# Optimization experiments

Hardware: AMD Instinct MI355X
Metric: run time of the kernel (lower is better)

The kernel has to match this reference:

```python
import jax, jax.numpy as jnp
import numpy as np

N_BATCH, S, CH = 16384, 7, 30  # B*5+num_classes = 2*5+20
CO_COORD, CO_NOOBJ = 5.0, 0.5


def setup_inputs() -> dict:
    key = jax.random.key(0)
    k1, k2, k3 = jax.random.split(key, 3)
    preds = jax.random.uniform(k1, (N_BATCH, S, S, CH), dtype=jnp.float32)
    targets = jax.random.uniform(k2, (N_BATCH, S, S, CH), dtype=jnp.float32)
    obj = (jax.random.uniform(k3, (N_BATCH, S, S)) > 0.7).astype(jnp.float32)
    targets = targets.at[..., 4].set(obj * targets[..., 4] + obj * 1e-3)
    return {"preds": preds, "targets": targets}


def reference(preds, targets):
    # NOTE: faithful to the original torch code, including its bug where
    # coo_target is taken from preds (so box_target/class_target == the
    # predictions), making loc_loss and class_loss identically zero while
    # contain_loss compares pred confidence against (detached) IoU.
    N = preds.shape[0]
    P = preds.reshape(-1, CH)            # [NC, 30], NC = N*S*S
    T = targets.reshape(-1, CH)
    conf_t = T[:, 4]
    coo = (conf_t > 0).astype(preds.dtype)   # cells with object
    noo = (conf_t == 0).astype(preds.dtype)  # cells without object

    # --- no-object confidence loss (channels 4 and 9) ---
    nooobj_loss = jnp.sum(noo * ((P[:, 4] - T[:, 4]) ** 2 + (P[:, 9] - T[:, 9]) ** 2))

    # --- per-cell box matching (vectorized version of the python loop) ---
    boxes = P[:, :10].reshape(-1, 2, 5)       # [NC, 2, 5] predicted boxes
    xy = boxes[..., :2] / 14.0                # 14.0 == 2*S hardcoded upstream
    wh = boxes[..., 2:4]
    lt1 = xy - 0.5 * wh                       # [NC, 2, 2]
    rb1 = xy + 0.5 * wh
    tbox = boxes[:, 0]                        # box2 = box_target[i] == first pred box (bug)
    lt2 = tbox[:, :2] / 14.0 - 0.5 * tbox[:, 2:4]  # [NC, 2]
    rb2 = tbox[:, :2] / 14.0 + 0.5 * tbox[:, 2:4]

    ilt = jnp.maximum(lt1, lt2[:, None, :])
    irb = jnp.minimum(rb1, rb2[:, None, :])
    iwh = jnp.maximum(irb - ilt, 0.0)
    inter = iwh[..., 0] * iwh[..., 1]                    # [NC, 2]
    area1 = (rb1 - lt1)[..., 0] * (rb1 - lt1)[..., 1]    # [NC, 2]
    area2 = ((rb2 - lt2)[..., 0] * (rb2 - lt2)[..., 1])[:, None]
    iou = inter / (area1 + area2 - inter)                # [NC, 2]

    max_iou = jnp.max(iou, axis=1)                       # [NC]
    idx = jnp.argmax(iou, axis=1)                        # [NC] in {0,1}
    resp = jnp.take_along_axis(boxes, idx[:, None, None], axis=1)[:, 0]       # responsible box
    nresp = jnp.take_along_axis(boxes, (1 - idx)[:, None, None], axis=1)[:, 0]
    tgt_resp = resp  # box_target == box_pred due to the upstream bug

    # contain: pred conf vs detached IoU (original uses max_iou.data)
    contain_loss = jnp.sum(coo * (resp[:, 4] - jax.lax.stop_gradient(max_iou)) ** 2)
    # loc: identically zero given the bug, but computed faithfully
    loc_loss = (jnp.sum(coo[:, None] * (resp[:, :2] - tgt_resp[:, :2]) ** 2)
                + jnp.sum(coo[:, None] * (jnp.sqrt(resp[:, 2:4]) - jnp.sqrt(tgt_resp[:, 2:4])) ** 2))
    # not-responsible box: target conf zeroed
    not_contain_loss = jnp.sum(coo * nresp[:, 4] ** 2)
    # class loss: class_target also taken from preds (bug) -> zero
    cls = P[:, 10:]
    class_loss = jnp.sum(coo[:, None] * (cls - cls) ** 2)

    total = (CO_COORD * loc_loss + contain_loss + CO_NOOBJ * not_contain_loss
             + CO_NOOBJ * nooobj_loss + class_loss) / N
    return total
```

## Files before the change

kernel.cpp:

```cpp
#include <hip/hip_runtime.h>


#define TILE 256
#define NT   2

__device__ __forceinline__ float cell_loss(const float p[10], float t4, float t9) {
    float coo = (t4 > 0.0f) ? 1.0f : 0.0f;
    float noo = (t4 == 0.0f) ? 1.0f : 0.0f;

    float d4 = p[4] - t4;
    float d9 = p[9] - t9;
    float noo_term = noo * (d4 * d4 + d9 * d9);

    float lt2x = p[0] / 14.0f - 0.5f * p[2];
    float lt2y = p[1] / 14.0f - 0.5f * p[3];
    float rb2x = p[0] / 14.0f + 0.5f * p[2];
    float rb2y = p[1] / 14.0f + 0.5f * p[3];
    float area2 = (rb2x - lt2x) * (rb2y - lt2y);

    float iou[2];
    #pragma unroll
    for (int b = 0; b < 2; ++b) {
        float x = p[5 * b] / 14.0f;
        float y = p[5 * b + 1] / 14.0f;
        float w = p[5 * b + 2];
        float h = p[5 * b + 3];
        float lt1x = x - 0.5f * w, lt1y = y - 0.5f * h;
        float rb1x = x + 0.5f * w, rb1y = y + 0.5f * h;
        float iltx = fmaxf(lt1x, lt2x), ilty = fmaxf(lt1y, lt2y);
        float irbx = fminf(rb1x, rb2x), irby = fminf(rb1y, rb2y);
        float iwx = fmaxf(irbx - iltx, 0.0f);
        float iwy = fmaxf(irby - ilty, 0.0f);
        float inter = iwx * iwy;
        float area1 = (rb1x - lt1x) * (rb1y - lt1y);
        iou[b] = inter / (area1 + area2 - inter);
    }

    int idx;
    float max_iou;
    if (isnan(iou[0]))      { idx = 0; max_iou = iou[0]; }
    else if (isnan(iou[1])) { idx = 1; max_iou = iou[1]; }
    else                    { idx = (iou[1] > iou[0]) ? 1 : 0;
                              max_iou = fmaxf(iou[0], iou[1]); }

    float resp4  = p[5 * idx + 4];
    float nresp4 = p[5 * (1 - idx) + 4];
    float cdiff  = resp4 - max_iou;
    return coo * (cdiff * cdiff + 0.5f * nresp4 * nresp4) + 0.5f * noo_term;
}

struct TileRegs { float4 pv[3]; float4 tv[2]; };

__device__ __forceinline__ void issue_tile(const float* __restrict__ preds,
                                           const float* __restrict__ targets,
                                           long tile0, int tid, TileRegs& R) {
    const float4* gp = reinterpret_cast<const float4*>(preds + tile0 * 30);
    const float4* gt = reinterpret_cast<const float4*>(targets + tile0 * 30);
    #pragma unroll
    for (int k = 0; k < 3; ++k) {
        int L = tid + 256 * k;
        int pair = L / 6, rr = L - pair * 6;
        int r = (rr < 3) ? rr : rr + 4;
        R.pv[k] = gp[pair * 15 + r];
    }
    #pragma unroll
    for (int k = 0; k < 2; ++k) {
        int L = tid + 256 * k;
        int pair = L / 4, rr = L & 3;
        int r = (rr < 2) ? rr + 1 : rr + 6;
        R.tv[k] = gt[pair * 15 + r];
    }
}

__device__ __forceinline__ void write_tile(float4* smem4, float2* S2, float* Tc,
                                           int tid, const TileRegs& R) {
    #pragma unroll
    for (int k = 0; k < 3; ++k) {
        int L = tid + 256 * k;
        int pair = L / 6, rr = L - pair * 6;
        if (rr == 2)      S2[(pair * 5 + 2) * 2]     = make_float2(R.pv[k].x, R.pv[k].y);
        else if (rr == 3) S2[(pair * 5 + 2) * 2 + 1] = make_float2(R.pv[k].z, R.pv[k].w);
        else { int slot = (rr < 2) ? rr : rr - 1; smem4[pair * 5 + slot] = R.pv[k]; }
    }
    #pragma unroll
    for (int k = 0; k < 2; ++k) {
        int L = tid + 256 * k;
        int pair = L / 4, rr = L & 3;
        float v = (rr == 0) ? R.tv[k].x : (rr == 1) ? R.tv[k].y
                : (rr == 2) ? R.tv[k].z : R.tv[k].w;
        Tc[pair * 4 + rr] = v;
    }
}

__device__ __forceinline__ float compute_tile(const float2* S2, const float* Tc, int tid) {
    float p[10];
    #pragma unroll
    for (int k = 0; k < 5; ++k) {
        float2 q = S2[5 * tid + k];
        p[2 * k]     = q.x;
        p[2 * k + 1] = q.y;
    }
    return cell_loss(p, Tc[2 * tid], Tc[2 * tid + 1]);
}

__global__ __launch_bounds__(256) void yolo_loss_kernel(
    const float* __restrict__ preds,
    const float* __restrict__ targets,
    float* __restrict__ partials,
    int ncells)
{
    __shared__ float4 smem4[768];
    __shared__ float  warp_sums[4];
    float2* S2 = reinterpret_cast<float2*>(smem4);
    float*  Tc = reinterpret_cast<float*>(smem4 + 640);

    const int tid = threadIdx.x;
    const long tA = (long)blockIdx.x * (NT * TILE);
    const long tB = tA + TILE;
    float contrib = 0.0f;

    if (tB + TILE <= ncells) {
        TileRegs A, B;
        issue_tile(preds, targets, tA, tid, A);
        write_tile(smem4, S2, Tc, tid, A);
        __syncthreads();
        issue_tile(preds, targets, tB, tid, B);
        contrib = compute_tile(S2, Tc, tid);
        __syncthreads();
        write_tile(smem4, S2, Tc, tid, B);
        __syncthreads();
        contrib += compute_tile(S2, Tc, tid);
    } else {
        #pragma unroll
        for (int t = 0; t < NT; ++t) {
            long cell = tA + (long)t * TILE + tid;
            if (cell < ncells) {
                long base = cell * 30;
                float p[10];
                #pragma unroll
                for (int k = 0; k < 5; ++k) {
                    float2 v = *reinterpret_cast<const float2*>(preds + base + 2 * k);
                    p[2 * k] = v.x;
                    p[2 * k + 1] = v.y;
                }
                contrib += cell_loss(p, targets[base + 4], targets[base + 9]);
            }
        }
    }

    #pragma unroll
    for (int off = 32; off > 0; off >>= 1)
        contrib += __shfl_down(contrib, off, 64);

    int lane = tid & 63;
    int wid  = tid >> 6;
    if (lane == 0) warp_sums[wid] = contrib;
    __syncthreads();

    if (tid == 0) {
        partials[blockIdx.x] = warp_sums[0] + warp_sums[1] + warp_sums[2] + warp_sums[3];
    }
}

__global__ __launch_bounds__(256) void yolo_reduce_kernel(
    const float* __restrict__ partials,
    float* __restrict__ out,
    int nparts)
{
    __shared__ float warp_sums[4];
    const int tid = threadIdx.x;

    float s = 0.0f;
    for (int i = tid; i < nparts; i += 256)
        s += partials[i];

    #pragma unroll
    for (int off = 32; off > 0; off >>= 1)
        s += __shfl_down(s, off, 64);

    int lane = tid & 63;
    int wid  = tid >> 6;
    if (lane == 0) warp_sums[wid] = s;
    __syncthreads();

    if (tid == 0) {
        out[0] = (warp_sums[0] + warp_sums[1] + warp_sums[2] + warp_sums[3])
                 * (1.0f / 16384.0f);
    }
}

extern "C" void kernel_launch(void* const* d_in, const int* in_sizes, int n_in,
                              void* d_out, int out_size, void* d_ws, size_t ws_size,
                              hipStream_t stream) {
    const float* preds   = (const float*)d_in[0];
    const float* targets = (const float*)d_in[1];
    float* out = (float*)d_out;
    float* partials = (float*)d_ws;

    int ncells = in_sizes[0] / 30;
    int grid = (ncells + NT * TILE - 1) / (NT * TILE);

    yolo_loss_kernel<<<grid, 256, 0, stream>>>(preds, targets, partials, ncells);
    yolo_reduce_kernel<<<1, 256, 0, stream>>>(partials, out, grid);
}
```

Baseline: 36.56 us.

## Stage tiles via direct global-to-LDS loads and issue both tiles upfront

Replaces the register-staged global loads and scattered LDS writes with `__builtin_amdgcn_global_load_lds` 16-byte transfers that land data in LDS in load order. Both tiles are now issued before a single barrier, and compute reads the raw interleaved layout with an even/odd-thread split. The goal is to cut VGPR staging, LDS write instructions and intermediate barriers while putting more loads in flight. In exchange, LDS use per block grows from about 12KB to 40KB, which can limit resident blocks per CU, and an extra barrier is added before the reduction reuses the shared buffer.

```diff
diff --git a/kernel.cpp b/kernel.cpp
--- a/kernel.cpp
+++ b/kernel.cpp
@@ -3,6 +3,13 @@
 
 #define TILE 256
 #define NT   2
+
+__device__ __forceinline__ void gld16(const void* g, void* lds) {
+    __builtin_amdgcn_global_load_lds(
+        (const __attribute__((address_space(1))) void*)g,
+        (__attribute__((address_space(3))) void*)lds,
+        16, 0, 0);
+}
 
 __device__ __forceinline__ float cell_loss(const float p[10], float t4, float t9) {
     float coo = (t4 > 0.0f) ? 1.0f : 0.0f;
@@ -49,58 +56,46 @@
     return coo * (cdiff * cdiff + 0.5f * nresp4 * nresp4) + 0.5f * noo_term;
 }
 
-struct TileRegs { float4 pv[3]; float4 tv[2]; };
-
-__device__ __forceinline__ void issue_tile(const float* __restrict__ preds,
-                                           const float* __restrict__ targets,
-                                           long tile0, int tid, TileRegs& R) {
-    const float4* gp = reinterpret_cast<const float4*>(preds + tile0 * 30);
-    const float4* gt = reinterpret_cast<const float4*>(targets + tile0 * 30);
+__device__ __forceinline__ void stage_tile(const float4* __restrict__ gp,
+                                           const float4* __restrict__ gt,
+                                           float4* ldsP, float4* ldsT, int tid) {
+    const int wid = tid >> 6;
     #pragma unroll
     for (int k = 0; k < 3; ++k) {
-        int L = tid + 256 * k;
+        int L = k * 256 + tid;
         int pair = L / 6, rr = L - pair * 6;
         int r = (rr < 3) ? rr : rr + 4;
-        R.pv[k] = gp[pair * 15 + r];
+        gld16(gp + pair * 15 + r, ldsP + k * 256 + wid * 64);
     }
     #pragma unroll
     for (int k = 0; k < 2; ++k) {
-        int L = tid + 256 * k;
-        int pair = L / 4, rr = L & 3;
+        int L = k * 256 + tid;
+        int pair = L >> 2, rr = L & 3;
         int r = (rr < 2) ? rr + 1 : rr + 6;
-        R.tv[k] = gt[pair * 15 + r];
+        gld16(gt + pair * 15 + r, ldsT + k * 256 + wid * 64);
     }
 }
 
-__device__ __forceinline__ void write_tile(float4* smem4, float2* S2, float* Tc,
-                                           int tid, const TileRegs& R) {
-    #pragma unroll
-    for (int k = 0; k < 3; ++k) {
-        int L = tid + 256 * k;
-        int pair = L / 6, rr = L - pair * 6;
-        if (rr == 2)      S2[(pair * 5 + 2) * 2]     = make_float2(R.pv[k].x, R.pv[k].y);
-        else if (rr == 3) S2[(pair * 5 + 2) * 2 + 1] = make_float2(R.pv[k].z, R.pv[k].w);
-        else { int slot = (rr < 2) ? rr : rr - 1; smem4[pair * 5 + slot] = R.pv[k]; }
+__device__ __forceinline__ float compute_tile(const float4* P, const float4* T, int tid) {
+    const int pr = tid >> 1;
+    float p[10];
+    if ((tid & 1) == 0) {
+        float4 a = P[6 * pr], b = P[6 * pr + 1], c = P[6 * pr + 2];
+        p[0]=a.x; p[1]=a.y; p[2]=a.z; p[3]=a.w;
+        p[4]=b.x; p[5]=b.y; p[6]=b.z; p[7]=b.w;
+        p[8]=c.x; p[9]=c.y;
+        float t4 = reinterpret_cast<const float*>(T + 4 * pr)[0];
+        float t9 = reinterpret_cast<const float*>(T + 4 * pr + 1)[1];
+        return cell_loss(p, t4, t9);
+    } else {
+        float4 a = P[6 * pr + 3], b = P[6 * pr + 4], c = P[6 * pr + 5];
+        p[0]=a.z; p[1]=a.w;
+        p[2]=b.x; p[3]=b.y; p[4]=b.z; p[5]=b.w;
+        p[6]=c.x; p[7]=c.y; p[8]=c.z; p[9]=c.w;
+        float t4 = reinterpret_cast<const float*>(T + 4 * pr + 2)[2];
+        float t9 = reinterpret_cast<const float*>(T + 4 * pr + 3)[3];
+        return cell_loss(p, t4, t9);
     }
-    #pragma unroll
-    for (int k = 0; k < 2; ++k) {
-        int L = tid + 256 * k;
-        int pair = L / 4, rr = L & 3;
-        float v = (rr == 0) ? R.tv[k].x : (rr == 1) ? R.tv[k].y
-                : (rr == 2) ? R.tv[k].z : R.tv[k].w;
-        Tc[pair * 4 + rr] = v;
-    }
-}
-
-__device__ __forceinline__ float compute_tile(const float2* S2, const float* Tc, int tid) {
-    float p[10];
-    #pragma unroll
-    for (int k = 0; k < 5; ++k) {
-        float2 q = S2[5 * tid + k];
-        p[2 * k]     = q.x;
-        p[2 * k + 1] = q.y;
-    }
-    return cell_loss(p, Tc[2 * tid], Tc[2 * tid + 1]);
 }
 
 __global__ __launch_bounds__(256) void yolo_loss_kernel(
@@ -109,10 +104,8 @@
     float* __restrict__ partials,
     int ncells)
 {
-    __shared__ float4 smem4[768];
-    __shared__ float  warp_sums[4];
-    float2* S2 = reinterpret_cast<float2*>(smem4);
-    float*  Tc = reinterpret_cast<float*>(smem4 + 640);
+    __shared__ float4 smem[2560];
+    float* warp_sums = reinterpret_cast<float*>(smem);
 
     const int tid = threadIdx.x;
     const long tA = (long)blockIdx.x * (NT * TILE);
@@ -120,16 +113,16 @@
     float contrib = 0.0f;
 
     if (tB + TILE <= ncells) {
-        TileRegs A, B;
-        issue_tile(preds, targets, tA, tid, A);
-        write_tile(smem4, S2, Tc, tid, A);
+        stage_tile(reinterpret_cast<const float4*>(preds + tA * 30),
+                   reinterpret_cast<const float4*>(targets + tA * 30),
+                   smem, smem + 768, tid);
+        stage_tile(reinterpret_cast<const float4*>(preds + tB * 30),
+                   reinterpret_cast<const float4*>(targets + tB * 30),
+                   smem + 1280, smem + 2048, tid);
         __syncthreads();
-        issue_tile(preds, targets, tB, tid, B);
-        contrib = compute_tile(S2, Tc, tid);
-        __syncthreads();
-        write_tile(smem4, S2, Tc, tid, B);
-        __syncthreads();
-        contrib += compute_tile(S2, Tc, tid);
+
+        contrib  = compute_tile(smem, smem + 768, tid);
+        contrib += compute_tile(smem + 1280, smem + 2048, tid);
     } else {
         #pragma unroll
         for (int t = 0; t < NT; ++t) {
@@ -154,6 +147,7 @@
 
     int lane = tid & 63;
     int wid  = tid >> 6;
+    __syncthreads();
     if (lane == 0) warp_sums[wid] = contrib;
     __syncthreads();
 
```

New measurement: 37.12 us. No clear change (+1.5%).
